# Kernel tuning notes

Measured on AMD Instinct MI355X. Metric: run time of the kernel, lower is better.

## Reference

```python
import jax, jax.numpy as jnp
import numpy as np

N = 20000      # nodes per side
E = 160000     # edges
C = 512        # input_channels
C_OUT = 512    # output_channels
TEMP = float(np.sqrt(C))  # self.temperature = sqrt(input_channels)
NEG_SLOPE = 0.01          # LeakyReLU default


def _xavier(key, shape):
    fan_in, fan_out = shape[1], shape[0]
    std = np.sqrt(2.0 / (fan_in + fan_out))
    return jax.random.normal(key, shape, dtype=jnp.float32) * std


def setup_inputs() -> dict:
    key = jax.random.key(0)
    ks = jax.random.split(key, 10)
    return {
        "node_left": jax.random.normal(ks[0], (N, C), dtype=jnp.float32),
        "segmentation_index_left": jax.random.randint(ks[1], (E,), 0, N),
        "index_left": jax.random.randint(ks[2], (E,), 0, N),
        "node_right": jax.random.normal(ks[3], (N, C), dtype=jnp.float32),
        "segmentation_index_right": jax.random.randint(ks[4], (E,), 0, N),
        "index_right": jax.random.randint(ks[5], (E,), 0, N),
        "Wk": _xavier(ks[6], (C, C)),      # key_projection.weight
        "Wv": _xavier(ks[7], (C, C)),      # value_projection.weight
        "Wo": _xavier(ks[8], (C_OUT, C)),  # out_projection Linear weight
        "bo": jnp.zeros((C_OUT,), dtype=jnp.float32),
    }


def segment_softmax(scores, seg_idx, num_segments, temperature):
    # numerically stable softmax over variable-length segments of edges
    s = scores / temperature
    m = jax.ops.segment_max(s, seg_idx, num_segments=num_segments)
    m = jnp.where(jnp.isneginf(m), 0.0, m)  # guard empty segments
    e = jnp.exp(s - m[seg_idx])
    z = jax.ops.segment_sum(e, seg_idx, num_segments=num_segments)
    return e / z[seg_idx]


def _message(translation, seg_idx, num_segments, neighbor, Wo, bo):
    attn = segment_softmax(translation, seg_idx, num_segments, TEMP)  # [E]
    # dropout is identity at inference
    msg = jax.ops.segment_sum(attn[:, None] * neighbor, seg_idx,
                              num_segments=num_segments)  # [N, C]
    h = msg @ Wo.T + bo
    return jnp.where(h >= 0, h, NEG_SLOPE * h)  # LeakyReLU


def reference(node_left, segmentation_index_left, index_left,
              node_right, segmentation_index_right, index_right,
              Wk, Wv, Wo, bo):
    n_left = node_left.shape[0]
    n_right = node_right.shape[0]
    # key projections gathered to edges
    left_center = (node_left @ Wk.T)[segmentation_index_left]    # [E, C]
    right_center = (node_right @ Wk.T)[segmentation_index_right]  # [E, C]
    # value projections gathered to edges (cross side)
    left_neighbor = (node_right @ Wv.T)[segmentation_index_right]  # [E, C]
    right_neighbor = (node_left @ Wv.T)[segmentation_index_left]   # [E, C]
    translation = jnp.sum(left_center * right_center, axis=1)      # [E]
    msg_left = _message(translation, segmentation_index_left, n_left,
                        left_neighbor, Wo, bo)
    msg_right = _message(translation, segmentation_index_right, n_right,
                         right_neighbor, Wo, bo)
    return (msg_left, msg_right)
```

## Files before the change

### kernel.cpp

```cpp
#include <hip/hip_runtime.h>


#define C_DIM 512
#define TEMP_INV (1.0f / 22.627416997969522f)

using bf16x8 = __attribute__((ext_vector_type(8))) __bf16;
using s16x8  = __attribute__((ext_vector_type(8))) short;
using s16x4  = __attribute__((ext_vector_type(4))) short;
using f32x4  = __attribute__((ext_vector_type(4))) float;

__device__ __forceinline__ float bf2f(short u) {
    union { unsigned u; float f; } t;
    t.u = ((unsigned)(unsigned short)u) << 16;
    return t.f;
}
__device__ __forceinline__ short f2bf(float f) {
    union { float f; unsigned u; } t;
    t.f = f;
    unsigned r = t.u + 0x7FFFu + ((t.u >> 16) & 1u);
    return (short)(r >> 16);
}

__global__ void cvt2_f32_bf16(const float* __restrict__ inA,
                              const float* __restrict__ inB,
                              short* __restrict__ out, long n4half) {
    long i = (long)blockIdx.x * blockDim.x + threadIdx.x;
    long stride = (long)gridDim.x * blockDim.x;
    long n4 = 2 * n4half;
    for (; i < n4; i += stride) {
        const float4* src = (i < n4half)
            ? reinterpret_cast<const float4*>(inA) + i
            : reinterpret_cast<const float4*>(inB) + (i - n4half);
        float4 v = *src;
        s16x4 o;
        o[0] = f2bf(v.x); o[1] = f2bf(v.y); o[2] = f2bf(v.z); o[3] = f2bf(v.w);
        reinterpret_cast<s16x4*>(out)[i] = o;
    }
}

__global__ void cvt_weights(const float* __restrict__ Wk,
                            const float* __restrict__ Wv,
                            const float* __restrict__ Wo,
                            short* __restrict__ Wkc, short* __restrict__ WoB,
                            short* __restrict__ WvT) {
    int b = blockIdx.x;
    int tid = threadIdx.x;
    if (b < 64) {
        __shared__ float t[64][65];
        int bx = b & 7, by = b >> 3;
#pragma unroll
        for (int i = 0; i < 4; ++i) {
            int idx = i * 256 + tid;
            int row = idx >> 4, c4 = idx & 15;
            float4 v = *(const float4*)&Wv[(size_t)(by * 64 + row) * 512 + bx * 64 + c4 * 4];
            t[row][c4 * 4 + 0] = v.x; t[row][c4 * 4 + 1] = v.y;
            t[row][c4 * 4 + 2] = v.z; t[row][c4 * 4 + 3] = v.w;
        }
        __syncthreads();
#pragma unroll
        for (int i = 0; i < 4; ++i) {
            int idx = i * 256 + tid;
            int row = idx >> 4, g = idx & 15;
            s16x4 o;
            o[0] = f2bf(t[g * 4 + 0][row]);
            o[1] = f2bf(t[g * 4 + 1][row]);
            o[2] = f2bf(t[g * 4 + 2][row]);
            o[3] = f2bf(t[g * 4 + 3][row]);
            *(s16x4*)&WvT[(size_t)(bx * 64 + row) * 512 + by * 64 + g * 4] = o;
        }
    } else {
        const float* src = (b < 128) ? Wk : Wo;
        short* dst = (b < 128) ? Wkc : WoB;
        long base = (long)(b & 63) * 1024;
#pragma unroll
        for (int i = 0; i < 4; ++i) {
            long idx = base + i * 256 + tid;
            float4 v = reinterpret_cast<const float4*>(src)[idx];
            s16x4 o;
            o[0] = f2bf(v.x); o[1] = f2bf(v.y); o[2] = f2bf(v.z); o[3] = f2bf(v.w);
            reinterpret_cast<s16x4*>(dst)[idx] = o;
        }
    }
}

__global__ __launch_bounds__(256, 4)
void gemm_bt(const short* __restrict__ A, const short* __restrict__ B,
             short* __restrict__ Cp, int M, int N, int K, int nn, int total) {
    __shared__ short As[2][128 * 32];
    __shared__ short Bs[2][128 * 32];

    const int bid = blockIdx.x;
    const int q = total >> 3, r = total & 7;
    const int xcd = bid & 7, idx = bid >> 3;
    const int swz = (xcd < r ? xcd * (q + 1) : r * (q + 1) + (xcd - r) * q) + idx;
    const int bm = (swz / nn) * 128;
    const int bn = (swz % nn) * 128;

    const int tid  = threadIdx.x;
    const int lane = tid & 63;
    const int wid  = tid >> 6;
    const int wm   = (wid >> 1) * 64;
    const int wn   = (wid & 1) * 64;
    const int lrow  = lane & 15;
    const int khalf = lane >> 4;

    auto stage = [&](short* dA, short* dB, int k0) {
#pragma unroll
        for (int j = 0; j < 2; ++j) {
            int L    = j * 256 + tid;
            int pr   = L >> 3;
            int slot = L & 7;
            int g    = slot ^ (pr & 7);
            int row  = pr * 2 + (g >> 2);
            int kg   = g & 3;
            int wb   = (j * 256 + (tid & ~63)) * 16;
            {
                int grow = bm + row; if (grow >= M) grow = M - 1;
                const short* src = A + (size_t)grow * K + k0 + kg * 8;
                __builtin_amdgcn_global_load_lds(
                    (__attribute__((address_space(1))) void*)src,
                    (__attribute__((address_space(3))) void*)((char*)dA + wb),
                    16, 0, 0);
            }
            {
                int grow = bn + row; if (grow >= N) grow = N - 1;
                const short* src = B + (size_t)grow * K + k0 + kg * 8;
                __builtin_amdgcn_global_load_lds(
                    (__attribute__((address_space(1))) void*)src,
                    (__attribute__((address_space(3))) void*)((char*)dB + wb),
                    16, 0, 0);
            }
        }
    };

    auto frag = [&](const short* h, int row) -> bf16x8 {
        int pr   = row >> 1;
        int g    = ((row & 1) << 2) | khalf;
        int slot = g ^ (pr & 7);
        return *(const bf16x8*)&h[pr * 64 + slot * 8];
    };

    f32x4 acc[4][4] = {};
    const int nt = K >> 5;

    stage(As[0], Bs[0], 0);

    for (int t = 0; t < nt; ++t) {
        const int cur = t & 1;
        if (t + 1 < nt) {
            stage(As[cur ^ 1], Bs[cur ^ 1], (t + 1) << 5);
            asm volatile("s_waitcnt vmcnt(4)" ::: "memory");
        } else {
            asm volatile("s_waitcnt vmcnt(0)" ::: "memory");
        }
        __builtin_amdgcn_s_barrier();

        const short* as = As[cur];
        const short* bs = Bs[cur];
        bf16x8 af[4], bfr[4];
#pragma unroll
        for (int m = 0; m < 4; ++m) af[m] = frag(as, wm + m * 16 + lrow);
#pragma unroll
        for (int n = 0; n < 4; ++n) bfr[n] = frag(bs, wn + n * 16 + lrow);

        asm volatile("s_waitcnt lgkmcnt(0)" ::: "memory");
        __builtin_amdgcn_sched_barrier(0);
        __builtin_amdgcn_s_barrier();

        __builtin_amdgcn_s_setprio(1);
#pragma unroll
        for (int m = 0; m < 4; ++m)
#pragma unroll
            for (int n = 0; n < 4; ++n)
                acc[m][n] = __builtin_amdgcn_mfma_f32_16x16x32_bf16(
                    af[m], bfr[n], acc[m][n], 0, 0, 0);
        __builtin_amdgcn_s_setprio(0);
    }

    const int crow0 = (lane >> 4) * 4;
    const int ccol  = lane & 15;
#pragma unroll
    for (int m = 0; m < 4; ++m) {
#pragma unroll
        for (int n = 0; n < 4; ++n) {
            int col = bn + wn + n * 16 + ccol;
#pragma unroll
            for (int r2 = 0; r2 < 4; ++r2) {
                int row = bm + wm + m * 16 + crow0 + r2;
                if (row < M) Cp[(size_t)row * N + col] = f2bf(acc[m][n][r2]);
            }
        }
    }
}

__global__ void edge_dot(const short* __restrict__ proj,
                         const int* __restrict__ segL, const int* __restrict__ segR,
                         float* __restrict__ w, int* __restrict__ cnt,
                         int E, int N) {
    int e0 = blockIdx.x * 16 + (threadIdx.x >> 6) * 4;
    if (e0 >= E) return;
    int lane = threadIdx.x & 63;

    int e[4];
    float sum[4];
#pragma unroll
    for (int k = 0; k < 4; ++k) {
        int ek = e0 + k;
        e[k] = (ek < E) ? ek : e0;
        const short* a = proj + (size_t)segL[e[k]] * 1024 + lane * 8;
        const short* b = proj + (size_t)(N + segR[e[k]]) * 1024 + lane * 8;
        s16x8 va = *(const s16x8*)a;
        s16x8 vb = *(const s16x8*)b;
        float s = 0.f;
#pragma unroll
        for (int j = 0; j < 8; ++j) s += bf2f(va[j]) * bf2f(vb[j]);
        sum[k] = s;
    }
#pragma unroll
    for (int o = 32; o > 0; o >>= 1) {
#pragma unroll
        for (int k = 0; k < 4; ++k) sum[k] += __shfl_xor(sum[k], o, 64);
    }
    if (lane < 4) {
        int ek = e0 + lane;
        if (ek < E) {
            float s = (lane == 0) ? sum[0] : (lane == 1) ? sum[1]
                    : (lane == 2) ? sum[2] : sum[3];
            w[ek] = __expf(s * TEMP_INV);
            atomicAdd(&cnt[segL[ek]], 1);
            atomicAdd(&cnt[N + segR[ek]], 1);
        }
    }
}

__global__ void scan_blocks(const int* __restrict__ cnt, int* __restrict__ off,
                            int* __restrict__ bsum, int n) {
    __shared__ int ws[4];
    int tid = threadIdx.x, lane = tid & 63, wid = tid >> 6;
    int i = blockIdx.x * 256 + tid;
    int x = (i < n) ? cnt[i] : 0;
    int v = x;
#pragma unroll
    for (int d = 1; d < 64; d <<= 1) {
        int t = __shfl_up(v, d, 64);
        if (lane >= d) v += t;
    }
    if (lane == 63) ws[wid] = v;
    __syncthreads();
    int woff = 0;
    for (int w = 0; w < wid; ++w) woff += ws[w];
    v += woff;
    if (i < n) off[i + 1] = v;
    if (tid == 255) bsum[blockIdx.x] = v;
}

__global__ void scan_tops(int* __restrict__ bsum, int nb) {
    __shared__ int ws[4];
    int tid = threadIdx.x, lane = tid & 63, wid = tid >> 6;
    int x = (tid < nb) ? bsum[tid] : 0;
    int v = x;
#pragma unroll
    for (int d = 1; d < 64; d <<= 1) {
        int t = __shfl_up(v, d, 64);
        if (lane >= d) v += t;
    }
    if (lane == 63) ws[wid] = v;
    __syncthreads();
    int woff = 0;
    for (int w = 0; w < wid; ++w) woff += ws[w];
    v += woff;
    if (tid < nb) bsum[tid] = v - x;
}

__global__ void scan_apply(int* __restrict__ off, const int* __restrict__ bsum,
                           int* __restrict__ cnt, int n) {
    int i = blockIdx.x * 256 + threadIdx.x;
    if (i < n) {
        off[i + 1] += bsum[blockIdx.x];
        cnt[i] = 0;
    }
    if (i == 0) off[0] = 0;
}

__global__ void fill_csr2(const int* __restrict__ segL, const int* __restrict__ segR,
                          const float* __restrict__ w,
                          const int* __restrict__ off, int* __restrict__ cur,
                          float2* __restrict__ pairs, int E, int N) {
    int i = blockIdx.x * blockDim.x + threadIdx.x;
    int st = gridDim.x * blockDim.x;
    for (; i < E; i += st) {
        int sl = segL[i], sr = segR[i];
        float we = w[i];
        int pl = off[sl] + atomicAdd(&cur[sl], 1);
        pairs[pl] = make_float2(we, __int_as_float(N + sr));
        int pr = off[N + sr] + atomicAdd(&cur[N + sr], 1);
        pairs[pr] = make_float2(we, __int_as_float(sl));
    }
}

__global__ void node_msg(const int* __restrict__ off,
                         const float2* __restrict__ pairs,
                         const short* __restrict__ proj,
                         const float* __restrict__ bo,
                         float* __restrict__ out, int NN2) {
    int n = blockIdx.x * 4 + (threadIdx.x >> 6);
    if (n >= NN2) return;
    int lane = threadIdx.x & 63;
    int beg = off[n], end = off[n + 1];
    const short* VW = proj + 512 + lane * 8;

    float acc[8] = {};
    float z = 0.f;
    int i = beg;
    for (; i + 3 < end; i += 4) {
        float2 p0 = pairs[i], p1 = pairs[i + 1];
        float2 p2 = pairs[i + 2], p3 = pairs[i + 3];
        const s16x8 v0 = *(const s16x8*)(VW + (size_t)__float_as_int(p0.y) * 1024);
        const s16x8 v1 = *(const s16x8*)(VW + (size_t)__float_as_int(p1.y) * 1024);
        const s16x8 v2 = *(const s16x8*)(VW + (size_t)__float_as_int(p2.y) * 1024);
        const s16x8 v3 = *(const s16x8*)(VW + (size_t)__float_as_int(p3.y) * 1024);
        z += (p0.x + p1.x) + (p2.x + p3.x);
#pragma unroll
        for (int j = 0; j < 8; ++j) {
            acc[j] += p0.x * bf2f(v0[j]) + p1.x * bf2f(v1[j]);
            acc[j] += p2.x * bf2f(v2[j]) + p3.x * bf2f(v3[j]);
        }
    }
    for (; i < end; ++i) {
        float2 p = pairs[i];
        const s16x8 v = *(const s16x8*)(VW + (size_t)__float_as_int(p.y) * 1024);
        z += p.x;
#pragma unroll
        for (int j = 0; j < 8; ++j) acc[j] += p.x * bf2f(v[j]);
    }
    float inv = (z > 0.f) ? 1.f / z : 0.f;

    float4 bs0 = *(const float4*)&bo[lane * 8];
    float4 bs1 = *(const float4*)&bo[lane * 8 + 4];
    float bb[8] = {bs0.x, bs0.y, bs0.z, bs0.w, bs1.x, bs1.y, bs1.z, bs1.w};
    float h[8];
#pragma unroll
    for (int j = 0; j < 8; ++j) {
        float v = acc[j] * inv + bb[j];
        h[j] = v >= 0.f ? v : 0.01f * v;
    }
    float* orow = out + (size_t)n * C_DIM + lane * 8;
    *(float4*)&orow[0] = make_float4(h[0], h[1], h[2], h[3]);
    *(float4*)&orow[4] = make_float4(h[4], h[5], h[6], h[7]);
}

extern "C" void kernel_launch(void* const* d_in, const int* in_sizes, int n_in,
                              void* d_out, int out_size, void* d_ws, size_t ws_size,
                              hipStream_t stream) {
    const float* node_left  = (const float*)d_in[0];
    const int*   segL       = (const int*)d_in[1];
    const float* node_right = (const float*)d_in[3];
    const int*   segR       = (const int*)d_in[4];
    const float* Wk         = (const float*)d_in[6];
    const float* Wv         = (const float*)d_in[7];
    const float* Wo         = (const float*)d_in[8];
    const float* bo         = (const float*)d_in[9];

    const int C = C_DIM;
    const int N = in_sizes[0] / C;
    const int E = in_sizes[1];
    const int NN2 = 2 * N;

    size_t offb = 0;
    auto alloc = [&](size_t bytes) -> void* {
        void* p = (char*)d_ws + offb;
        offb += (bytes + 255) & ~(size_t)255;
        return p;
    };
    short* nodeLR_b = (short*)alloc((size_t)NN2 * C * 2);
    short* Wkc_b  = (short*)alloc((size_t)1024 * C * 2);
    short* Wc_b   = Wkc_b + (size_t)C * C;
    short* Wo_b   = (short*)alloc((size_t)C * C * 2);
    short* WvT_b  = (short*)alloc((size_t)C * C * 2);
    short* proj   = (short*)alloc((size_t)NN2 * 1024 * 2);
    float* w_arr  = (float*)alloc((size_t)E * 4);
    float2* pairs = (float2*)alloc((size_t)2 * E * 8);
    int* cnt  = (int*)alloc((size_t)NN2 * 4);
    int* off  = (int*)alloc((size_t)(NN2 + 1) * 4);
    int* bsum = (int*)alloc(256 * 4);

    const int nsb = (NN2 + 255) / 256;

    hipMemsetAsync(cnt, 0, (size_t)NN2 * 4, stream);
    cvt2_f32_bf16<<<2048, 256, 0, stream>>>(node_left, node_right, nodeLR_b,
                                            (long)N * C / 4);
    cvt_weights<<<192, 256, 0, stream>>>(Wk, Wv, Wo, Wkc_b, Wo_b, WvT_b);

    gemm_bt<<<16, 256, 0, stream>>>(Wo_b, WvT_b, Wc_b, C, C, C, 4, 16);
    {
        int nm = (NN2 + 127) / 128, nn = 1024 / 128;
        int total = nm * nn;
        gemm_bt<<<total, 256, 0, stream>>>(nodeLR_b, Wkc_b, proj, NN2, 1024, C,
                                           nn, total);
    }

    edge_dot<<<(E + 15) / 16, 256, 0, stream>>>(proj, segL, segR, w_arr, cnt, E, N);

    scan_blocks<<<nsb, 256, 0, stream>>>(cnt, off, bsum, NN2);
    scan_tops<<<1, 256, 0, stream>>>(bsum, nsb);
    scan_apply<<<nsb, 256, 0, stream>>>(off, bsum, cnt, NN2);
    fill_csr2<<<512, 256, 0, stream>>>(segL, segR, w_arr, off, cnt, pairs, E, N);

    node_msg<<<(NN2 + 3) / 4, 256, 0, stream>>>(off, pairs, proj, bo,
                                                (float*)d_out, NN2);
}
```

Before: 222.4 us.

## Triple-buffer GEMM, fuse edge dot into CSR fill, nontemporal output stores

The GEMM moves from double to triple-buffered LDS staging, prefetching two K-tiles ahead, and its launch bound drops from 4 to 3 blocks per SM to make room. Edge counting and the prefix scan now run before the GEMMs using only the segment indices, so the edge dot-product kernel can write the exp weights straight into CSR pairs. This drops the intermediate weight array and the separate fill kernel. The final output uses nontemporal stores, and the fused path keeps atomic slot assignment, so edge order within a node stays nondeterministic.

```diff
diff --git a/kernel.cpp b/kernel.cpp
--- a/kernel.cpp
+++ b/kernel.cpp
@@ -83,11 +83,11 @@
     }
 }
 
-__global__ __launch_bounds__(256, 4)
+__global__ __launch_bounds__(256, 3)
 void gemm_bt(const short* __restrict__ A, const short* __restrict__ B,
              short* __restrict__ Cp, int M, int N, int K, int nn, int total) {
-    __shared__ short As[2][128 * 32];
-    __shared__ short Bs[2][128 * 32];
+    __shared__ short As[3][128 * 32];
+    __shared__ short Bs[3][128 * 32];
 
     const int bid = blockIdx.x;
     const int q = total >> 3, r = total & 7;
@@ -144,11 +144,15 @@
     const int nt = K >> 5;
 
     stage(As[0], Bs[0], 0);
+    stage(As[1], Bs[1], 32);
 
     for (int t = 0; t < nt; ++t) {
-        const int cur = t & 1;
-        if (t + 1 < nt) {
-            stage(As[cur ^ 1], Bs[cur ^ 1], (t + 1) << 5);
+        const unsigned cur = (unsigned)t % 3u;
+        if (t + 2 < nt) {
+            const unsigned nxt = (unsigned)(t + 2) % 3u;
+            stage(As[nxt], Bs[nxt], (t + 2) << 5);
+            asm volatile("s_waitcnt vmcnt(8)" ::: "memory");
+        } else if (t + 1 < nt) {
             asm volatile("s_waitcnt vmcnt(4)" ::: "memory");
         } else {
             asm volatile("s_waitcnt vmcnt(0)" ::: "memory");
@@ -193,43 +197,13 @@
     }
 }
 
-__global__ void edge_dot(const short* __restrict__ proj,
-                         const int* __restrict__ segL, const int* __restrict__ segR,
-                         float* __restrict__ w, int* __restrict__ cnt,
-                         int E, int N) {
-    int e0 = blockIdx.x * 16 + (threadIdx.x >> 6) * 4;
-    if (e0 >= E) return;
-    int lane = threadIdx.x & 63;
-
-    int e[4];
-    float sum[4];
-#pragma unroll
-    for (int k = 0; k < 4; ++k) {
-        int ek = e0 + k;
-        e[k] = (ek < E) ? ek : e0;
-        const short* a = proj + (size_t)segL[e[k]] * 1024 + lane * 8;
-        const short* b = proj + (size_t)(N + segR[e[k]]) * 1024 + lane * 8;
-        s16x8 va = *(const s16x8*)a;
-        s16x8 vb = *(const s16x8*)b;
-        float s = 0.f;
-#pragma unroll
-        for (int j = 0; j < 8; ++j) s += bf2f(va[j]) * bf2f(vb[j]);
-        sum[k] = s;
-    }
-#pragma unroll
-    for (int o = 32; o > 0; o >>= 1) {
-#pragma unroll
-        for (int k = 0; k < 4; ++k) sum[k] += __shfl_xor(sum[k], o, 64);
-    }
-    if (lane < 4) {
-        int ek = e0 + lane;
-        if (ek < E) {
-            float s = (lane == 0) ? sum[0] : (lane == 1) ? sum[1]
-                    : (lane == 2) ? sum[2] : sum[3];
-            w[ek] = __expf(s * TEMP_INV);
-            atomicAdd(&cnt[segL[ek]], 1);
-            atomicAdd(&cnt[N + segR[ek]], 1);
-        }
+__global__ void count_edges2(const int* __restrict__ segL, const int* __restrict__ segR,
+                             int* __restrict__ cnt, int E, int N) {
+    int i = blockIdx.x * blockDim.x + threadIdx.x;
+    int st = gridDim.x * blockDim.x;
+    for (; i < E; i += st) {
+        atomicAdd(&cnt[segL[i]], 1);
+        atomicAdd(&cnt[N + segR[i]], 1);
     }
 }
 
@@ -282,19 +256,44 @@
     if (i == 0) off[0] = 0;
 }
 
-__global__ void fill_csr2(const int* __restrict__ segL, const int* __restrict__ segR,
-                          const float* __restrict__ w,
-                          const int* __restrict__ off, int* __restrict__ cur,
-                          float2* __restrict__ pairs, int E, int N) {
-    int i = blockIdx.x * blockDim.x + threadIdx.x;
-    int st = gridDim.x * blockDim.x;
-    for (; i < E; i += st) {
-        int sl = segL[i], sr = segR[i];
-        float we = w[i];
-        int pl = off[sl] + atomicAdd(&cur[sl], 1);
-        pairs[pl] = make_float2(we, __int_as_float(N + sr));
-        int pr = off[N + sr] + atomicAdd(&cur[N + sr], 1);
-        pairs[pr] = make_float2(we, __int_as_float(sl));
+__global__ void edge_dot_fill(const short* __restrict__ proj,
+                              const int* __restrict__ segL, const int* __restrict__ segR,
+                              const int* __restrict__ off, int* __restrict__ cur,
+                              float2* __restrict__ pairs, int E, int N) {
+    int e0 = blockIdx.x * 16 + (threadIdx.x >> 6) * 4;
+    if (e0 >= E) return;
+    int lane = threadIdx.x & 63;
+
+    float sum[4];
+#pragma unroll
+    for (int k = 0; k < 4; ++k) {
+        int ek = e0 + k; if (ek >= E) ek = e0;
+        const short* a = proj + (size_t)segL[ek] * 1024 + lane * 8;
+        const short* b = proj + (size_t)(N + segR[ek]) * 1024 + lane * 8;
+        s16x8 va = *(const s16x8*)a;
+        s16x8 vb = *(const s16x8*)b;
+        float s = 0.f;
+#pragma unroll
+        for (int j = 0; j < 8; ++j) s += bf2f(va[j]) * bf2f(vb[j]);
+        sum[k] = s;
+    }
+#pragma unroll
+    for (int o = 32; o > 0; o >>= 1) {
+#pragma unroll
+        for (int k = 0; k < 4; ++k) sum[k] += __shfl_xor(sum[k], o, 64);
+    }
+    if (lane < 4) {
+        int ek = e0 + lane;
+        if (ek < E) {
+            float s = (lane == 0) ? sum[0] : (lane == 1) ? sum[1]
+                    : (lane == 2) ? sum[2] : sum[3];
+            float we = __expf(s * TEMP_INV);
+            int sl = segL[ek], sr = segR[ek];
+            int pl = off[sl] + atomicAdd(&cur[sl], 1);
+            pairs[pl] = make_float2(we, __int_as_float(N + sr));
+            int pr = off[N + sr] + atomicAdd(&cur[N + sr], 1);
+            pairs[pr] = make_float2(we, __int_as_float(sl));
+        }
     }
 }
 
@@ -338,15 +337,20 @@
     float4 bs0 = *(const float4*)&bo[lane * 8];
     float4 bs1 = *(const float4*)&bo[lane * 8 + 4];
     float bb[8] = {bs0.x, bs0.y, bs0.z, bs0.w, bs1.x, bs1.y, bs1.z, bs1.w};
-    float h[8];
-#pragma unroll
-    for (int j = 0; j < 8; ++j) {
+    f32x4 h0, h1;
+#pragma unroll
+    for (int j = 0; j < 4; ++j) {
         float v = acc[j] * inv + bb[j];
-        h[j] = v >= 0.f ? v : 0.01f * v;
+        h0[j] = v >= 0.f ? v : 0.01f * v;
+    }
+#pragma unroll
+    for (int j = 0; j < 4; ++j) {
+        float v = acc[4 + j] * inv + bb[4 + j];
+        h1[j] = v >= 0.f ? v : 0.01f * v;
     }
     float* orow = out + (size_t)n * C_DIM + lane * 8;
-    *(float4*)&orow[0] = make_float4(h[0], h[1], h[2], h[3]);
-    *(float4*)&orow[4] = make_float4(h[4], h[5], h[6], h[7]);
+    __builtin_nontemporal_store(h0, (f32x4*)&orow[0]);
+    __builtin_nontemporal_store(h1, (f32x4*)&orow[4]);
 }
 
 extern "C" void kernel_launch(void* const* d_in, const int* in_sizes, int n_in,
@@ -378,7 +382,6 @@
     short* Wo_b   = (short*)alloc((size_t)C * C * 2);
     short* WvT_b  = (short*)alloc((size_t)C * C * 2);
     short* proj   = (short*)alloc((size_t)NN2 * 1024 * 2);
-    float* w_arr  = (float*)alloc((size_t)E * 4);
     float2* pairs = (float2*)alloc((size_t)2 * E * 8);
     int* cnt  = (int*)alloc((size_t)NN2 * 4);
     int* off  = (int*)alloc((size_t)(NN2 + 1) * 4);
@@ -387,6 +390,11 @@
     const int nsb = (NN2 + 255) / 256;
 
     hipMemsetAsync(cnt, 0, (size_t)NN2 * 4, stream);
+    count_edges2<<<512, 256, 0, stream>>>(segL, segR, cnt, E, N);
+    scan_blocks<<<nsb, 256, 0, stream>>>(cnt, off, bsum, NN2);
+    scan_tops<<<1, 256, 0, stream>>>(bsum, nsb);
+    scan_apply<<<nsb, 256, 0, stream>>>(off, bsum, cnt, NN2);
+
     cvt2_f32_bf16<<<2048, 256, 0, stream>>>(node_left, node_right, nodeLR_b,
                                             (long)N * C / 4);
     cvt_weights<<<192, 256, 0, stream>>>(Wk, Wv, Wo, Wkc_b, Wo_b, WvT_b);
@@ -399,12 +407,8 @@
                                            nn, total);
     }
 
-    edge_dot<<<(E + 15) / 16, 256, 0, stream>>>(proj, segL, segR, w_arr, cnt, E, N);
-
-    scan_blocks<<<nsb, 256, 0, stream>>>(cnt, off, bsum, NN2);
-    scan_tops<<<1, 256, 0, stream>>>(bsum, nsb);
-    scan_apply<<<nsb, 256, 0, stream>>>(off, bsum, cnt, NN2);
-    fill_csr2<<<512, 256, 0, stream>>>(segL, segR, w_arr, off, cnt, pairs, E, N);
+    edge_dot_fill<<<(E + 15) / 16, 256, 0, stream>>>(proj, segL, segR, off, cnt,
+                                                     pairs, E, N);
 
     node_msg<<<(NN2 + 3) / 4, 256, 0, stream>>>(off, pairs, proj, bo,
                                                 (float*)d_out, NN2);
```

Result: slower. 230.1 us (+3.5%).
